# Kernel tuning notes

Hardware: AMD Instinct MI355X
Metric: run time of the kernel (lower is better)

The kernel has to match this reference:

```python
import jax, jax.numpy as jnp
import numpy as np
from jax import lax

K = 3  # kernel_size
S = 2  # stride


def setup_inputs() -> dict:
    key = jax.random.key(0)
    k1, k2 = jax.random.split(key)
    # NHWC input, matching the TF layer's layout
    x = jax.random.normal(k1, (8, 128, 128, 128), dtype=jnp.float32)
    # one [K,K,1,1] deconv kernel per channel, stacked -> [K,K,1,C]
    w = jax.random.normal(k2, (K, K, 1, 128), dtype=jnp.float32) * 0.1
    return {"x": x, "w": w}


def reference(x, w):
    """Channel-wise (depthwise) transposed conv, SAME padding, out = in*S.

    Equivalent to TF conv2d_transpose applied per channel: expressed as a
    single fractionally-strided conv (lhs_dilation=S) with the spatially
    flipped kernel and feature_group_count=C (no cross-channel mixing).
    """
    C = x.shape[-1]
    w_flipped = w[::-1, ::-1]  # conv_transpose == dilated conv with flipped kernel
    # forward SAME-conv padding (output=in*S down to in): total = K - S (K >= S)
    pf = K - S
    pf_lo, pf_hi = pf // 2, pf - pf // 2
    # transpose padding: (K-1) - forward padding on each side
    pad = (K - 1 - pf_lo, K - 1 - pf_hi)
    out = lax.conv_general_dilated(
        x, w_flipped,
        window_strides=(1, 1),
        padding=(pad, pad),
        lhs_dilation=(S, S),
        dimension_numbers=("NHWC", "HWIO", "NHWC"),
        feature_group_count=C,
    )  # [N, H*S, W*S, C]
    return out
```

## Files before the change

kernel.cpp:

```cpp
#include <hip/hip_runtime.h>


typedef float v4f __attribute__((ext_vector_type(4)));

__global__ __launch_bounds__(256) void upsample_tconv_kernel(
    const float* __restrict__ x, const float* __restrict__ w,
    float* __restrict__ out)
{
    int idx = blockIdx.x * blockDim.x + threadIdx.x;
    int c4 = idx & 31;
    int tg = (idx >> 5) & 31;
    int y  = (idx >> 10) & 127;
    int n  = idx >> 17;

    const v4f* wv = (const v4f*)w;
    v4f w00 = wv[0 * 32 + c4];
    v4f w01 = wv[1 * 32 + c4];
    v4f w02 = wv[2 * 32 + c4];
    v4f w10 = wv[3 * 32 + c4];
    v4f w11 = wv[4 * 32 + c4];
    v4f w12 = wv[5 * 32 + c4];
    v4f w20 = wv[6 * 32 + c4];
    v4f w21 = wv[7 * 32 + c4];
    v4f w22 = wv[8 * 32 + c4];

    const v4f zero = (v4f)(0.f);
    const v4f* xv = (const v4f*)x;

    int t0 = tg << 2;
    int rowbase = ((n * 128 + y) * 128) * 32 + c4;
    int upbase  = rowbase - 128 * 32;
    bool has_up = (y > 0);

    v4f xpa = (t0 > 0) ? xv[rowbase + (t0 - 1) * 32] : zero;
    v4f xpc = (has_up && t0 > 0) ? xv[upbase + (t0 - 1) * 32] : zero;

    v4f* ov = (v4f*)out;
    int oy = y << 1;
    int ob0 = ((n * 256 + oy) * 256 + (t0 << 1)) * 32 + c4;
    int ob1 = ob0 + 256 * 32;

    #pragma unroll
    for (int k = 0; k < 4; ++k) {
        v4f xa = xv[rowbase + (t0 + k) * 32];
        v4f xc = has_up ? xv[upbase + (t0 + k) * 32] : zero;

        v4f o_ee = w00 * xa + w02 * xpa + w20 * xc + w22 * xpc;
        v4f o_eo = w01 * xa + w21 * xc;
        v4f o_oe = w10 * xa + w12 * xpa;
        v4f o_oo = w11 * xa;

        int o = ob0 + (k << 1) * 32;
        ov[o] = o_ee;
        ov[o + 32] = o_eo;
        o = ob1 + (k << 1) * 32;
        ov[o] = o_oe;
        ov[o + 32] = o_oo;

        xpa = xa;
        xpc = xc;
    }
}

extern "C" void kernel_launch(void* const* d_in, const int* in_sizes, int n_in,
                              void* d_out, int out_size, void* d_ws, size_t ws_size,
                              hipStream_t stream) {
    const float* x = (const float*)d_in[0];
    const float* w = (const float*)d_in[1];
    float* out = (float*)d_out;

    upsample_tconv_kernel<<<dim3(4096), dim3(256), 0, stream>>>(x, w, out);
}
```

Baseline: 321.6 us.

## Tile four input rows per thread and use nontemporal output stores

Each thread now handles a 4x4 input tile instead of a 1x4 strip. Rows are kept in registers so every input row is loaded once and reused as the upper neighbour of the next row, which cuts redundant global reads of x. Output writes use nontemporal stores to avoid polluting the cache with the large write-only stream. The grid shrinks by four, leaving fewer waves to hide memory latency, and register pressure rises.

```diff
diff --git a/kernel.cpp b/kernel.cpp
--- a/kernel.cpp
+++ b/kernel.cpp
@@ -10,8 +10,8 @@
     int idx = blockIdx.x * blockDim.x + threadIdx.x;
     int c4 = idx & 31;
     int tg = (idx >> 5) & 31;
-    int y  = (idx >> 10) & 127;
-    int n  = idx >> 17;
+    int yb = (idx >> 10) & 31;
+    int n  = idx >> 15;
 
     const v4f* wv = (const v4f*)w;
     v4f w00 = wv[0 * 32 + c4];
@@ -26,40 +26,55 @@
 
     const v4f zero = (v4f)(0.f);
     const v4f* xv = (const v4f*)x;
+    v4f* ov = (v4f*)out;
 
     int t0 = tg << 2;
-    int rowbase = ((n * 128 + y) * 128) * 32 + c4;
-    int upbase  = rowbase - 128 * 32;
-    bool has_up = (y > 0);
+    int y0 = yb << 2;
+    bool lh = (t0 > 0);
+    int rb = ((n * 128 + y0) * 128 + t0) * 32 + c4;
+    int ob = ((n * 256 + (y0 << 1)) * 256 + (t0 << 1)) * 32 + c4;
 
-    v4f xpa = (t0 > 0) ? xv[rowbase + (t0 - 1) * 32] : zero;
-    v4f xpc = (has_up && t0 > 0) ? xv[upbase + (t0 - 1) * 32] : zero;
+#define LOADROW(H, R0, R1, R2, R3, base) \
+    do { int _b = (base); \
+         H  = lh ? xv[_b - 32] : zero; \
+         R0 = xv[_b];       R1 = xv[_b + 32]; \
+         R2 = xv[_b + 64];  R3 = xv[_b + 96]; } while (0)
 
-    v4f* ov = (v4f*)out;
-    int oy = y << 1;
-    int ob0 = ((n * 256 + oy) * 256 + (t0 << 1)) * 32 + c4;
-    int ob1 = ob0 + 256 * 32;
+#define KCOL(XA, XPA, XC, XPC, OO) \
+    do { __builtin_nontemporal_store(w00*(XA) + w02*(XPA) + w20*(XC) + w22*(XPC), &ov[_o  + (OO)*32]); \
+         __builtin_nontemporal_store(w01*(XA) + w21*(XC),                          &ov[_o  + ((OO)+1)*32]); \
+         __builtin_nontemporal_store(w10*(XA) + w12*(XPA),                         &ov[_o2 + (OO)*32]); \
+         __builtin_nontemporal_store(w11*(XA),                                     &ov[_o2 + ((OO)+1)*32]); } while (0)
 
-    #pragma unroll
-    for (int k = 0; k < 4; ++k) {
-        v4f xa = xv[rowbase + (t0 + k) * 32];
-        v4f xc = has_up ? xv[upbase + (t0 + k) * 32] : zero;
+#define ROW(AH, A0, A1, A2, A3, CH, C0, C1, C2, C3, OB) \
+    do { int _o = (OB); int _o2 = _o + 8192; \
+         KCOL(A0, AH, C0, CH, 0); \
+         KCOL(A1, A0, C1, C0, 2); \
+         KCOL(A2, A1, C2, C1, 4); \
+         KCOL(A3, A2, C3, C2, 6); } while (0)
 
-        v4f o_ee = w00 * xa + w02 * xpa + w20 * xc + w22 * xpc;
-        v4f o_eo = w01 * xa + w21 * xc;
-        v4f o_oe = w10 * xa + w12 * xpa;
-        v4f o_oo = w11 * xa;
+    v4f ch, c0, c1, c2, c3;
+    if (y0 > 0) {
+        LOADROW(ch, c0, c1, c2, c3, rb - 4096);
+    } else {
+        ch = zero; c0 = zero; c1 = zero; c2 = zero; c3 = zero;
+    }
+    v4f ah, a0, a1, a2, a3;
+    LOADROW(ah, a0, a1, a2, a3, rb);
 
-        int o = ob0 + (k << 1) * 32;
-        ov[o] = o_ee;
-        ov[o + 32] = o_eo;
-        o = ob1 + (k << 1) * 32;
-        ov[o] = o_oe;
-        ov[o + 32] = o_oo;
+    v4f nh, n0, n1, n2, n3;
 
-        xpa = xa;
-        xpc = xc;
-    }
+    LOADROW(nh, n0, n1, n2, n3, rb + 4096);
+    ROW(ah, a0, a1, a2, a3, ch, c0, c1, c2, c3, ob);
+    LOADROW(ch, c0, c1, c2, c3, rb + 2 * 4096);
+    ROW(nh, n0, n1, n2, n3, ah, a0, a1, a2, a3, ob + 2 * 8192);
+    LOADROW(ah, a0, a1, a2, a3, rb + 3 * 4096);
+    ROW(ch, c0, c1, c2, c3, nh, n0, n1, n2, n3, ob + 4 * 8192);
+    ROW(ah, a0, a1, a2, a3, ch, c0, c1, c2, c3, ob + 6 * 8192);
+
+#undef ROW
+#undef KCOL
+#undef LOADROW
 }
 
 extern "C" void kernel_launch(void* const* d_in, const int* in_sizes, int n_in,
@@ -69,5 +84,5 @@
     const float* w = (const float*)d_in[1];
     float* out = (float*)d_out;
 
-    upsample_tconv_kernel<<<dim3(4096), dim3(256), 0, stream>>>(x, w, out);
+    upsample_tconv_kernel<<<dim3(1024), dim3(256), 0, stream>>>(x, w, out);
 }
```

Result: faster. 312.8 us (-2.7%).

## Remap threads so each block covers half a row, with nontemporal stores

Applied to the files above, without the earlier changes.

Each block now handles half of one input row. Within a block, the 8 column-groups of threads interleave columns, so every loop iteration writes contiguous output across the block, and each thread handles 8 columns instead of 4 consecutive ones. The left-neighbour values are reloaded instead of carried in registers, which adds redundant loads that should mostly hit in cache. Output writes use nontemporal stores to avoid polluting the cache with the large write-only output, and the grid is halved to 2048 blocks with an occupancy hint in launch_bounds.

```diff
diff --git a/kernel.cpp b/kernel.cpp
--- a/kernel.cpp
+++ b/kernel.cpp
@@ -3,15 +3,18 @@
 
 typedef float v4f __attribute__((ext_vector_type(4)));
 
-__global__ __launch_bounds__(256) void upsample_tconv_kernel(
+__global__ __launch_bounds__(256, 4) void upsample_tconv_kernel(
     const float* __restrict__ x, const float* __restrict__ w,
     float* __restrict__ out)
 {
-    int idx = blockIdx.x * blockDim.x + threadIdx.x;
-    int c4 = idx & 31;
-    int tg = (idx >> 5) & 31;
-    int y  = (idx >> 10) & 127;
-    int n  = idx >> 17;
+    int b = blockIdx.x;
+    int seg = b & 1;
+    int y   = (b >> 1) & 127;
+    int n   = b >> 8;
+
+    int tid  = threadIdx.x;
+    int c4   = tid & 31;
+    int tcol = tid >> 5;
 
     const v4f* wv = (const v4f*)w;
     v4f w00 = wv[0 * 32 + c4];
@@ -26,39 +29,32 @@
 
     const v4f zero = (v4f)(0.f);
     const v4f* xv = (const v4f*)x;
+    v4f* ov = (v4f*)out;
 
-    int t0 = tg << 2;
-    int rowbase = ((n * 128 + y) * 128) * 32 + c4;
-    int upbase  = rowbase - 128 * 32;
     bool has_up = (y > 0);
-
-    v4f xpa = (t0 > 0) ? xv[rowbase + (t0 - 1) * 32] : zero;
-    v4f xpc = (has_up && t0 > 0) ? xv[upbase + (t0 - 1) * 32] : zero;
-
-    v4f* ov = (v4f*)out;
-    int oy = y << 1;
-    int ob0 = ((n * 256 + oy) * 256 + (t0 << 1)) * 32 + c4;
-    int ob1 = ob0 + 256 * 32;
+    int rowb  = ((n * 128 + y) * 128) * 32 + c4;
+    int obrow = ((n * 256 + (y << 1)) * 256) * 32 + c4;
+    int tb = (seg << 6) + tcol;
 
     #pragma unroll
-    for (int k = 0; k < 4; ++k) {
-        v4f xa = xv[rowbase + (t0 + k) * 32];
-        v4f xc = has_up ? xv[upbase + (t0 + k) * 32] : zero;
+    for (int k = 0; k < 8; ++k) {
+        int t = tb + (k << 3);
+        int base = rowb + t * 32;
+        v4f xa  = xv[base];
+        v4f xpa = (t > 0) ? xv[base - 32] : zero;
+        v4f xc  = has_up ? xv[base - 128 * 32] : zero;
+        v4f xpc = (has_up && t > 0) ? xv[base - 128 * 32 - 32] : zero;
 
         v4f o_ee = w00 * xa + w02 * xpa + w20 * xc + w22 * xpc;
         v4f o_eo = w01 * xa + w21 * xc;
         v4f o_oe = w10 * xa + w12 * xpa;
         v4f o_oo = w11 * xa;
 
-        int o = ob0 + (k << 1) * 32;
-        ov[o] = o_ee;
-        ov[o + 32] = o_eo;
-        o = ob1 + (k << 1) * 32;
-        ov[o] = o_oe;
-        ov[o + 32] = o_oo;
-
-        xpa = xa;
-        xpc = xc;
+        int ob = obrow + (t << 1) * 32;
+        __builtin_nontemporal_store(o_ee, &ov[ob]);
+        __builtin_nontemporal_store(o_eo, &ov[ob + 32]);
+        __builtin_nontemporal_store(o_oe, &ov[ob + 256 * 32]);
+        __builtin_nontemporal_store(o_oo, &ov[ob + 256 * 32 + 32]);
     }
 }
 
@@ -69,5 +65,5 @@
     const float* w = (const float*)d_in[1];
     float* out = (float*)d_out;
 
-    upsample_tconv_kernel<<<dim3(4096), dim3(256), 0, stream>>>(x, w, out);
+    upsample_tconv_kernel<<<dim3(2048), dim3(256), 0, stream>>>(x, w, out);
 }
```

Result: no change. 316.1 us (median of 2 runs) (-1.7%).
